# Optimization experiments

Hardware: AMD Instinct MI355X
Metric: run time of the kernel (lower is better)

## Reference

```python
import jax, jax.numpy as jnp
import numpy as np
from jax.scipy.linalg import expm

N = 2048

def setup_inputs() -> dict:
    key = jax.random.key(0)
    # Learnable parameter A, initialized as 0.01 * randn(n, n) per the module's __init__.
    A = 0.01 * jax.random.normal(key, (N, N), dtype=jnp.float32)
    return {"A": A}

def reference(A) -> jnp.ndarray:
    # S = A - A^T is skew-symmetric, so expm(S) lies in SO(n).
    S = A - A.T
    return expm(S)
```

## Files before the change

### kernel.cpp

```cpp
#include <hip/hip_runtime.h>
#include <stdint.h>

#define NM 2048

typedef _Float16 f16;
typedef __attribute__((ext_vector_type(8))) _Float16 half8;
typedef __attribute__((ext_vector_type(4))) float float4v;

__global__ void skew_f16_kernel(const float* __restrict__ A, f16* __restrict__ X) {
    __shared__ float t[32][33];
    const int bx = blockIdx.x * 32, by = blockIdx.y * 32;
    const int tx = threadIdx.x, ty = threadIdx.y;
    #pragma unroll
    for (int r = 0; r < 32; r += 8)
        t[ty + r][tx] = A[(size_t)(bx + ty + r) * NM + by + tx];
    __syncthreads();
    #pragma unroll
    for (int r = 0; r < 32; r += 8) {
        const int i = by + ty + r, j = bx + tx;
        X[(size_t)i * NM + j] = (f16)(A[(size_t)i * NM + j] - t[tx][ty + r]);
    }
}

template <int MODE>
__global__ __launch_bounds__(512, 4) void gemm_ps_kernel(
    const f16* __restrict__ Ap, const f16* __restrict__ BT,
    const f16* __restrict__ Xp, f16* __restrict__ X2p,
    f16* __restrict__ CTp, float* __restrict__ OUT) {
    constexpr int PLA = 128 * 64;
    constexpr int PLB = 64 * 64;
    constexpr int BUFH = PLA + PLB;
    constexpr int STAGEB = 2 * BUFH * 2;
    constexpr int MERGEB = 4 * 2176 * 4;
    constexpr int SMB = STAGEB > MERGEB ? STAGEB : MERGEB;
    __shared__ __align__(16) char smem_raw[SMB];

    const int tid = threadIdx.x;
    const int wave = tid >> 6, lane = tid & 63;
    const int grp = wave >> 2, w4 = wave & 3;
    const int wr = w4 >> 1, wc = w4 & 1;
    const int l15 = lane & 15, qq = lane >> 4;

    const int bid = blockIdx.x;
    const int xcd = bid & 7, li = bid >> 3;
    const int by = (xcd >> 2) * 8 + (li >> 3);
    const int bx = (xcd & 3) * 8 + (li & 7);
    const int rowBase = by * 128, colBase = bx * 64;

    const f16* gsrc[3];
    int ldsoff[3];
    #pragma unroll
    for (int u = 0; u < 3; ++u) {
        const int c = (u < 2) ? (u * 512 + tid) : tid;
        const int m = c >> 3, sp = c & 7;
        const int sl = sp ^ (m & 7);
        if (u < 2) {
            ldsoff[u] = c * 8;
            gsrc[u] = Ap + (size_t)(rowBase + m) * NM + sl * 8;
        } else {
            ldsoff[u] = PLA + c * 8;
            gsrc[u] = BT + (size_t)(colBase + m) * NM + sl * 8;
        }
    }

    int offA[4], offB[2];
    #pragma unroll
    for (int r = 0; r < 4; ++r) {
        const int m = wr * 64 + r * 16 + l15;
        offA[r] = (m * 8 + ((grp * 4 + qq) ^ (m & 7))) * 8;
    }
    #pragma unroll
    for (int c = 0; c < 2; ++c) {
        const int n = wc * 32 + c * 16 + l15;
        offB[c] = PLA + (n * 8 + ((grp * 4 + qq) ^ (n & 7))) * 8;
    }

    float4v acc[4][2];
    #pragma unroll
    for (int r = 0; r < 4; ++r)
        #pragma unroll
        for (int c = 0; c < 2; ++c)
            acc[r][c] = (float4v){0.f, 0.f, 0.f, 0.f};

    auto stage = [&](int buf) {
        f16* base = (f16*)smem_raw + buf * BUFH;
        #pragma unroll
        for (int u = 0; u < 3; ++u) {
            __builtin_amdgcn_global_load_lds(
                (const __attribute__((address_space(1))) void*)gsrc[u],
                (__attribute__((address_space(3))) void*)(uintptr_t)(base + ldsoff[u]),
                16, 0, 0);
            gsrc[u] += 64;
        }
    };

    stage(0);
    for (int k = 0; k < 32; ++k) {
        __syncthreads();
        if (k < 31) stage((k + 1) & 1);
        const f16* base = (const f16*)smem_raw + (k & 1) * BUFH;
        half8 ah[4], bh[2];
        #pragma unroll
        for (int r = 0; r < 4; ++r) ah[r] = *(const half8*)&base[offA[r]];
        #pragma unroll
        for (int c = 0; c < 2; ++c) bh[c] = *(const half8*)&base[offB[c]];
        #pragma unroll
        for (int r = 0; r < 4; ++r)
            #pragma unroll
            for (int c = 0; c < 2; ++c)
                acc[r][c] = __builtin_amdgcn_mfma_f32_16x16x32_f16(ah[r], bh[c], acc[r][c], 0, 0, 0);
    }

    __syncthreads();
    float* mbuf = (float*)smem_raw;
    if (wave >= 4) {
        float* base = mbuf + (size_t)w4 * 2176;
        #pragma unroll
        for (int r = 0; r < 4; ++r)
            #pragma unroll
            for (int c = 0; c < 2; ++c) {
                const int off = (c * 16 + l15) * 68 + r * 16 + qq * 4;
                *(float4v*)&base[off] = acc[r][c];
            }
    }
    __syncthreads();
    if (wave < 4) {
        const float* base = mbuf + (size_t)w4 * 2176;
        #pragma unroll
        for (int r = 0; r < 4; ++r)
            #pragma unroll
            for (int c = 0; c < 2; ++c) {
                const int off = (c * 16 + l15) * 68 + r * 16 + qq * 4;
                acc[r][c] += *(const float4v*)&base[off];
            }
        #pragma unroll
        for (int r = 0; r < 4; ++r)
            #pragma unroll
            for (int c = 0; c < 2; ++c)
                #pragma unroll
                for (int g = 0; g < 4; ++g) {
                    const int row = rowBase + wr * 64 + r * 16 + qq * 4 + g;
                    const int col = colBase + wc * 32 + c * 16 + l15;
                    const size_t off = (size_t)row * NM + col;
                    float v = acc[r][c][g];
                    if (MODE == 0) {
                        v = -v;
                        const float x = (float)Xp[off];
                        X2p[off] = (f16)v;
                        CTp[off] = (f16)(v * (256.0f / 24.0f) - x * (256.0f / 6.0f));
                    } else {
                        const float x = (float)Xp[off];
                        const float x2 = (float)X2p[off];
                        float o = x + 0.5f * x2 + v * (1.0f / 256.0f);
                        if (row == col) o += 1.0f;
                        OUT[off] = o;
                    }
                }
    }
}

extern "C" void kernel_launch(void* const* d_in, const int* in_sizes, int n_in,
                              void* d_out, int out_size, void* d_ws, size_t ws_size,
                              hipStream_t stream) {
    const float* A = (const float*)d_in[0];
    float* out = (float*)d_out;
    const size_t NN = (size_t)NM * NM;

    f16* X  = (f16*)d_ws;
    f16* X2 = X + NN;
    f16* CT = X2 + NN;

    dim3 tb(32, 8);
    dim3 tg(NM / 32, NM / 32);

    skew_f16_kernel<<<tg, tb, 0, stream>>>(A, X);
    gemm_ps_kernel<0><<<512, 512, 0, stream>>>(X, X, X, X2, CT, nullptr);
    gemm_ps_kernel<1><<<512, 512, 0, stream>>>(X2, CT, X, X2, nullptr, out);
}
```

Measured before the change: 124.0 us.

## Use 256x256 split-K GEMM tiles with partial sums and separate reduce kernels

New measurement: 136.2 us. +9.8%, slower.

```diff
diff --git a/kernel.cpp b/kernel.cpp
--- a/kernel.cpp
+++ b/kernel.cpp
@@ -22,141 +22,220 @@
     }
 }
 
-template <int MODE>
-__global__ __launch_bounds__(512, 4) void gemm_ps_kernel(
-    const f16* __restrict__ Ap, const f16* __restrict__ BT,
-    const f16* __restrict__ Xp, f16* __restrict__ X2p,
-    f16* __restrict__ CTp, float* __restrict__ OUT) {
-    constexpr int PLA = 128 * 64;
-    constexpr int PLB = 64 * 64;
-    constexpr int BUFH = PLA + PLB;
-    constexpr int STAGEB = 2 * BUFH * 2;
-    constexpr int MERGEB = 4 * 2176 * 4;
-    constexpr int SMB = STAGEB > MERGEB ? STAGEB : MERGEB;
-    __shared__ __align__(16) char smem_raw[SMB];
-
-    const int tid = threadIdx.x;
+#define STAGE_UNIT(kt, u)                                                         \
+    {                                                                             \
+        f16* _b = lds + ((kt) & 1) * BUFH;                                        \
+        const f16* _g = gsrc[u] + (kt) * 64;                                      \
+        __builtin_amdgcn_global_load_lds(                                         \
+            (const __attribute__((address_space(1))) void*)_g,                    \
+            (__attribute__((address_space(3))) void*)(uintptr_t)(_b + loff[u]),   \
+            16, 0, 0);                                                            \
+        __builtin_amdgcn_global_load_lds(                                         \
+            (const __attribute__((address_space(1))) void*)(_g + (size_t)128 * NM), \
+            (__attribute__((address_space(3))) void*)(uintptr_t)(_b + loff[u] + 8192), \
+            16, 0, 0);                                                            \
+    }
+
+#define MFMA_QUAD(MH, NH)                                                         \
+    __builtin_amdgcn_s_setprio(1);                                                \
+    _Pragma("unroll")                                                             \
+    for (int r = 0; r < 4; ++r)                                                   \
+        _Pragma("unroll")                                                         \
+        for (int c = 0; c < 2; ++c)                                               \
+            _Pragma("unroll")                                                     \
+            for (int kk = 0; kk < 2; ++kk)                                        \
+                acc[MH][NH][r][c] = __builtin_amdgcn_mfma_f32_16x16x32_f16(       \
+                    ah[r][kk], bh[c][kk], acc[MH][NH][r][c], 0, 0, 0);            \
+    __builtin_amdgcn_s_setprio(0);                                                \
+    asm volatile("s_waitcnt lgkmcnt(0)" ::: "memory");                            \
+    asm volatile("s_barrier" ::: "memory");
+
+__global__ __launch_bounds__(512, 2) void gemm8_kernel(
+    const f16* __restrict__ Ap, const f16* __restrict__ BTp, f16* __restrict__ Pp)
+{
+    extern __shared__ __align__(16) f16 lds[];
+    constexpr int PLB  = 16384;
+    constexpr int BUFH = 32768;
+    constexpr int NT   = 8;
+
+    const int tid  = threadIdx.x;
     const int wave = tid >> 6, lane = tid & 63;
-    const int grp = wave >> 2, w4 = wave & 3;
-    const int wr = w4 >> 1, wc = w4 & 1;
+    const int wr = wave >> 2, wc = wave & 3;
     const int l15 = lane & 15, qq = lane >> 4;
 
     const int bid = blockIdx.x;
     const int xcd = bid & 7, li = bid >> 3;
-    const int by = (xcd >> 2) * 8 + (li >> 3);
-    const int bx = (xcd & 3) * 8 + (li & 7);
-    const int rowBase = by * 128, colBase = bx * 64;
-
-    const f16* gsrc[3];
-    int ldsoff[3];
-    #pragma unroll
-    for (int u = 0; u < 3; ++u) {
-        const int c = (u < 2) ? (u * 512 + tid) : tid;
-        const int m = c >> 3, sp = c & 7;
-        const int sl = sp ^ (m & 7);
-        if (u < 2) {
-            ldsoff[u] = c * 8;
-            gsrc[u] = Ap + (size_t)(rowBase + m) * NM + sl * 8;
-        } else {
-            ldsoff[u] = PLA + c * 8;
-            gsrc[u] = BT + (size_t)(colBase + m) * NM + sl * 8;
+    const int sk   = xcd >> 1;
+    const int trow = (xcd & 1) * 4 + (li >> 3);
+    const int tcol = li & 7;
+    const int rowBase = trow * 256, colBase = tcol * 256;
+    const int kBase = sk * 512;
+
+    const f16* gsrc[4];
+    int loff[4];
+    {
+        const int m = tid >> 3, sp = tid & 7;
+        const int rA0 = m;
+        const int rA1 = 64 + m;
+        const int rB0 = (m & 31) + ((m >> 5) << 6);
+        const int rB1 = 32 + rB0;
+        gsrc[0] = Ap  + (size_t)(rowBase + rA0) * NM + kBase + (sp ^ (rA0 & 7)) * 8;
+        gsrc[1] = Ap  + (size_t)(rowBase + rA1) * NM + kBase + (sp ^ (rA1 & 7)) * 8;
+        gsrc[2] = BTp + (size_t)(colBase + rB0) * NM + kBase + (sp ^ (rB0 & 7)) * 8;
+        gsrc[3] = BTp + (size_t)(colBase + rB1) * NM + kBase + (sp ^ (rB1 & 7)) * 8;
+        loff[0] = (rA0 * 8 + sp) * 8;
+        loff[1] = (rA1 * 8 + sp) * 8;
+        loff[2] = PLB + (rB0 * 8 + sp) * 8;
+        loff[3] = PLB + (rB1 * 8 + sp) * 8;
+    }
+
+    int offA[4][2], offB[2][2];
+    #pragma unroll
+    for (int r = 0; r < 4; ++r)
+        #pragma unroll
+        for (int kk = 0; kk < 2; ++kk) {
+            const int row = wr * 128 + r * 16 + l15;
+            offA[r][kk] = (row * 8 + ((kk * 4 + qq) ^ (row & 7))) * 8;
         }
-    }
-
-    int offA[4], offB[2];
-    #pragma unroll
-    for (int r = 0; r < 4; ++r) {
-        const int m = wr * 64 + r * 16 + l15;
-        offA[r] = (m * 8 + ((grp * 4 + qq) ^ (m & 7))) * 8;
-    }
-    #pragma unroll
-    for (int c = 0; c < 2; ++c) {
-        const int n = wc * 32 + c * 16 + l15;
-        offB[c] = PLA + (n * 8 + ((grp * 4 + qq) ^ (n & 7))) * 8;
-    }
-
-    float4v acc[4][2];
-    #pragma unroll
-    for (int r = 0; r < 4; ++r)
+    #pragma unroll
+    for (int c = 0; c < 2; ++c)
+        #pragma unroll
+        for (int kk = 0; kk < 2; ++kk) {
+            const int row = wc * 64 + c * 16 + l15;
+            offB[c][kk] = PLB + (row * 8 + ((kk * 4 + qq) ^ (row & 7))) * 8;
+        }
+
+    float4v acc[2][2][4][2];
+    #pragma unroll
+    for (int mh = 0; mh < 2; ++mh)
+        #pragma unroll
+        for (int nh = 0; nh < 2; ++nh)
+            #pragma unroll
+            for (int r = 0; r < 4; ++r)
+                #pragma unroll
+                for (int c = 0; c < 2; ++c)
+                    acc[mh][nh][r][c] = (float4v){0.f, 0.f, 0.f, 0.f};
+
+    half8 ah[4][2], bh[2][2];
+
+    STAGE_UNIT(0, 0)
+    STAGE_UNIT(0, 3)
+    STAGE_UNIT(0, 1)
+    STAGE_UNIT(0, 2)
+    STAGE_UNIT(1, 0)
+    STAGE_UNIT(1, 3)
+
+    #pragma unroll
+    for (int t = 0; t < NT; ++t) {
+        const f16* base = lds + (t & 1) * BUFH;
+
+        if (t + 1 < NT) STAGE_UNIT(t + 1, 1)
+        if (t == NT - 1) { asm volatile("s_waitcnt vmcnt(0)" ::: "memory"); }
+        else             { asm volatile("s_waitcnt vmcnt(6)" ::: "memory"); }
+        asm volatile("s_barrier" ::: "memory");
+        #pragma unroll
+        for (int r = 0; r < 4; ++r)
+            #pragma unroll
+            for (int kk = 0; kk < 2; ++kk)
+                ah[r][kk] = *(const half8*)&base[offA[r][kk]];
         #pragma unroll
         for (int c = 0; c < 2; ++c)
-            acc[r][c] = (float4v){0.f, 0.f, 0.f, 0.f};
-
-    auto stage = [&](int buf) {
-        f16* base = (f16*)smem_raw + buf * BUFH;
-        #pragma unroll
-        for (int u = 0; u < 3; ++u) {
-            __builtin_amdgcn_global_load_lds(
-                (const __attribute__((address_space(1))) void*)gsrc[u],
-                (__attribute__((address_space(3))) void*)(uintptr_t)(base + ldsoff[u]),
-                16, 0, 0);
-            gsrc[u] += 64;
-        }
-    };
-
-    stage(0);
-    for (int k = 0; k < 32; ++k) {
-        __syncthreads();
-        if (k < 31) stage((k + 1) & 1);
-        const f16* base = (const f16*)smem_raw + (k & 1) * BUFH;
-        half8 ah[4], bh[2];
-        #pragma unroll
-        for (int r = 0; r < 4; ++r) ah[r] = *(const half8*)&base[offA[r]];
-        #pragma unroll
-        for (int c = 0; c < 2; ++c) bh[c] = *(const half8*)&base[offB[c]];
+            #pragma unroll
+            for (int kk = 0; kk < 2; ++kk)
+                bh[c][kk] = *(const half8*)&base[offB[c][kk]];
+        MFMA_QUAD(0, 0)
+
+        if (t + 1 < NT) STAGE_UNIT(t + 1, 2)
+        asm volatile("s_barrier" ::: "memory");
+        #pragma unroll
+        for (int c = 0; c < 2; ++c)
+            #pragma unroll
+            for (int kk = 0; kk < 2; ++kk)
+                bh[c][kk] = *(const half8*)&base[offB[c][kk] + 2048];
+        MFMA_QUAD(0, 1)
+
+        if (t + 2 < NT) STAGE_UNIT(t + 2, 0)
+        asm volatile("s_barrier" ::: "memory");
         #pragma unroll
         for (int r = 0; r < 4; ++r)
             #pragma unroll
-            for (int c = 0; c < 2; ++c)
-                acc[r][c] = __builtin_amdgcn_mfma_f32_16x16x32_f16(ah[r], bh[c], acc[r][c], 0, 0, 0);
-    }
-
-    __syncthreads();
-    float* mbuf = (float*)smem_raw;
-    if (wave >= 4) {
-        float* base = mbuf + (size_t)w4 * 2176;
-        #pragma unroll
-        for (int r = 0; r < 4; ++r)
-            #pragma unroll
-            for (int c = 0; c < 2; ++c) {
-                const int off = (c * 16 + l15) * 68 + r * 16 + qq * 4;
-                *(float4v*)&base[off] = acc[r][c];
-            }
-    }
-    __syncthreads();
-    if (wave < 4) {
-        const float* base = mbuf + (size_t)w4 * 2176;
-        #pragma unroll
-        for (int r = 0; r < 4; ++r)
-            #pragma unroll
-            for (int c = 0; c < 2; ++c) {
-                const int off = (c * 16 + l15) * 68 + r * 16 + qq * 4;
-                acc[r][c] += *(const float4v*)&base[off];
-            }
-        #pragma unroll
-        for (int r = 0; r < 4; ++r)
-            #pragma unroll
-            for (int c = 0; c < 2; ++c)
+            for (int kk = 0; kk < 2; ++kk)
+                ah[r][kk] = *(const half8*)&base[offA[r][kk] + 4096];
+        MFMA_QUAD(1, 1)
+
+        if (t + 2 < NT) STAGE_UNIT(t + 2, 3)
+        asm volatile("s_barrier" ::: "memory");
+        #pragma unroll
+        for (int c = 0; c < 2; ++c)
+            #pragma unroll
+            for (int kk = 0; kk < 2; ++kk)
+                bh[c][kk] = *(const half8*)&base[offB[c][kk]];
+        MFMA_QUAD(1, 0)
+    }
+
+    f16* dst = Pp + (size_t)sk * NM * NM;
+    #pragma unroll
+    for (int mh = 0; mh < 2; ++mh)
+        #pragma unroll
+        for (int nh = 0; nh < 2; ++nh)
+            #pragma unroll
+            for (int r = 0; r < 4; ++r)
                 #pragma unroll
-                for (int g = 0; g < 4; ++g) {
-                    const int row = rowBase + wr * 64 + r * 16 + qq * 4 + g;
-                    const int col = colBase + wc * 32 + c * 16 + l15;
-                    const size_t off = (size_t)row * NM + col;
-                    float v = acc[r][c][g];
-                    if (MODE == 0) {
-                        v = -v;
-                        const float x = (float)Xp[off];
-                        X2p[off] = (f16)v;
-                        CTp[off] = (f16)(v * (256.0f / 24.0f) - x * (256.0f / 6.0f));
-                    } else {
-                        const float x = (float)Xp[off];
-                        const float x2 = (float)X2p[off];
-                        float o = x + 0.5f * x2 + v * (1.0f / 256.0f);
-                        if (row == col) o += 1.0f;
-                        OUT[off] = o;
+                for (int c = 0; c < 2; ++c)
+                    #pragma unroll
+                    for (int g = 0; g < 4; ++g) {
+                        const int row = rowBase + wr * 128 + mh * 64 + r * 16 + qq * 4 + g;
+                        const int col = colBase + wc * 64 + nh * 32 + c * 16 + l15;
+                        dst[(size_t)row * NM + col] = (f16)acc[mh][nh][r][c][g];
                     }
-                }
-    }
+}
+
+__global__ __launch_bounds__(256) void reduce0_kernel(
+    const f16* __restrict__ P, const f16* __restrict__ X,
+    f16* __restrict__ X2, f16* __restrict__ CT)
+{
+    const size_t NN = (size_t)NM * NM;
+    const size_t i = ((size_t)blockIdx.x * 256 + threadIdx.x) * 8;
+    const half8 p0 = *(const half8*)(P + i);
+    const half8 p1 = *(const half8*)(P + NN + i);
+    const half8 p2 = *(const half8*)(P + 2 * NN + i);
+    const half8 p3 = *(const half8*)(P + 3 * NN + i);
+    const half8 xv = *(const half8*)(X + i);
+    half8 x2v, ctv;
+    #pragma unroll
+    for (int j = 0; j < 8; ++j) {
+        const float s  = (float)p0[j] + (float)p1[j] + (float)p2[j] + (float)p3[j];
+        const float x2 = -s;
+        const float x  = (float)xv[j];
+        x2v[j] = (f16)x2;
+        ctv[j] = (f16)(x2 * (256.0f / 24.0f) - x * (256.0f / 6.0f));
+    }
+    *(half8*)(X2 + i) = x2v;
+    *(half8*)(CT + i) = ctv;
+}
+
+__global__ __launch_bounds__(256) void reduce1_kernel(
+    const f16* __restrict__ P, const f16* __restrict__ X,
+    const f16* __restrict__ X2, float* __restrict__ OUT)
+{
+    const size_t NN = (size_t)NM * NM;
+    const size_t i = ((size_t)blockIdx.x * 256 + threadIdx.x) * 8;
+    const half8 p0  = *(const half8*)(P + i);
+    const half8 p1  = *(const half8*)(P + NN + i);
+    const half8 p2  = *(const half8*)(P + 2 * NN + i);
+    const half8 p3  = *(const half8*)(P + 3 * NN + i);
+    const half8 xv  = *(const half8*)(X + i);
+    const half8 x2v = *(const half8*)(X2 + i);
+    float o[8];
+    #pragma unroll
+    for (int j = 0; j < 8; ++j) {
+        const float q = (float)p0[j] + (float)p1[j] + (float)p2[j] + (float)p3[j];
+        o[j] = (float)xv[j] + 0.5f * (float)x2v[j] + q * (1.0f / 256.0f);
+    }
+    const int row = (int)(i >> 11), col0 = (int)(i & 2047);
+    if (row >= col0 && row < col0 + 8) o[row - col0] += 1.0f;
+    *(float4v*)(OUT + i)     = (float4v){o[0], o[1], o[2], o[3]};
+    *(float4v*)(OUT + i + 4) = (float4v){o[4], o[5], o[6], o[7]};
 }
 
 extern "C" void kernel_launch(void* const* d_in, const int* in_sizes, int n_in,
@@ -169,11 +248,19 @@
     f16* X  = (f16*)d_ws;
     f16* X2 = X + NN;
     f16* CT = X2 + NN;
-
-    dim3 tb(32, 8);
-    dim3 tg(NM / 32, NM / 32);
-
+    f16* P  = CT + NN;
+
+    static int attr_done = 0;
+    if (!attr_done) {
+        hipFuncSetAttribute((const void*)gemm8_kernel,
+                            hipFuncAttributeMaxDynamicSharedMemorySize, 131072);
+        attr_done = 1;
+    }
+
+    dim3 tb(32, 8), tg(NM / 32, NM / 32);
     skew_f16_kernel<<<tg, tb, 0, stream>>>(A, X);
-    gemm_ps_kernel<0><<<512, 512, 0, stream>>>(X, X, X, X2, CT, nullptr);
-    gemm_ps_kernel<1><<<512, 512, 0, stream>>>(X2, CT, X, X2, nullptr, out);
-}
+    gemm8_kernel<<<256, 512, 131072, stream>>>(X, X, P);
+    reduce0_kernel<<<2048, 256, 0, stream>>>(P, X, X2, CT);
+    gemm8_kernel<<<256, 512, 131072, stream>>>(X2, CT, P);
+    reduce1_kernel<<<2048, 256, 0, stream>>>(P, X, X2, out);
+}
```

## Restructure GEMM to 128x128 tiles with explicit half-tile LDS pipelining

Applied to the files above, without the earlier changes.

Measured after the change: 122.7 us. No clear change (-1.1%).

```diff
diff --git a/kernel.cpp b/kernel.cpp
--- a/kernel.cpp
+++ b/kernel.cpp
@@ -22,141 +22,172 @@
     }
 }
 
+#define BARRIER asm volatile("s_barrier" ::: "memory")
+#define LG0     asm volatile("s_waitcnt lgkmcnt(0)" ::: "memory")
+#define W3      asm volatile("s_waitcnt vmcnt(3)" ::: "memory")
+#define W0      asm volatile("s_waitcnt vmcnt(0)" ::: "memory")
+#define NOST    ((void)0)
+
+#define STAGE_1(u, dst)                                                       \
+    do {                                                                      \
+        __builtin_amdgcn_global_load_lds(                                     \
+            (const __attribute__((address_space(1))) void*)gsrc[u],           \
+            (__attribute__((address_space(3))) void*)(uintptr_t)((dst) + loff[u]), \
+            16, 0, 0);                                                        \
+        gsrc[u] += 64;                                                        \
+    } while (0)
+
+#define RD_A(BB, HOFF)                                                       \
+    { _Pragma("unroll")                                                      \
+      for (int r_ = 0; r_ < 2; ++r_)                                         \
+        _Pragma("unroll")                                                    \
+        for (int k_ = 0; k_ < 2; ++k_)                                       \
+            ah[r_][k_] = *(const half8*)&(BB)[offA[r_][k_] + (HOFF)]; }
+
+#define RD_B(BB)                                                             \
+    { _Pragma("unroll")                                                      \
+      for (int c_ = 0; c_ < 2; ++c_)                                         \
+        _Pragma("unroll")                                                    \
+        for (int k_ = 0; k_ < 2; ++k_)                                       \
+            bh[c_][k_] = *(const half8*)&(BB)[offB[c_][k_]]; }
+
+#define MPH(MH)                                                              \
+    __builtin_amdgcn_s_setprio(1);                                           \
+    _Pragma("unroll")                                                        \
+    for (int r_ = 0; r_ < 2; ++r_)                                           \
+        _Pragma("unroll")                                                    \
+        for (int c_ = 0; c_ < 2; ++c_)                                       \
+            _Pragma("unroll")                                                 \
+            for (int k_ = 0; k_ < 2; ++k_)                                   \
+                acc[MH][r_][c_] = __builtin_amdgcn_mfma_f32_16x16x32_f16(    \
+                    ah[r_][k_], bh[c_][k_], acc[MH][r_][c_], 0, 0, 0);       \
+    __builtin_amdgcn_s_setprio(0);
+
+#define TILE2(CUR, S1, S2, WEND)                                             \
+    {                                                                        \
+        const f16* Bb = (CUR);                                               \
+                                                  \
+        RD_A(Bb, 0); RD_B(Bb);                                               \
+        S1;                                                                  \
+        BARRIER; LG0;                                                        \
+        MPH(0);                                                              \
+        BARRIER;                                                             \
+                                  \
+        RD_A(Bb, 2048);                                                      \
+        S2;                                                                  \
+        BARRIER; LG0;                                                        \
+        MPH(1);                                                              \
+        WEND; BARRIER;                                                       \
+    }
+
 template <int MODE>
-__global__ __launch_bounds__(512, 4) void gemm_ps_kernel(
-    const f16* __restrict__ Ap, const f16* __restrict__ BT,
+__global__ __launch_bounds__(512, 1) void gemm_fused_kernel(
+    const f16* __restrict__ Ap, const f16* __restrict__ BTp,
     const f16* __restrict__ Xp, f16* __restrict__ X2p,
-    f16* __restrict__ CTp, float* __restrict__ OUT) {
-    constexpr int PLA = 128 * 64;
-    constexpr int PLB = 64 * 64;
-    constexpr int BUFH = PLA + PLB;
-    constexpr int STAGEB = 2 * BUFH * 2;
-    constexpr int MERGEB = 4 * 2176 * 4;
-    constexpr int SMB = STAGEB > MERGEB ? STAGEB : MERGEB;
-    __shared__ __align__(16) char smem_raw[SMB];
-
-    const int tid = threadIdx.x;
+    f16* __restrict__ CTp, float* __restrict__ OUT)
+{
+    extern __shared__ __align__(16) f16 lds[];
+    constexpr int PLB  = 8192;
+    constexpr int BUFH = 16384;
+
+    const int tid  = threadIdx.x;
     const int wave = tid >> 6, lane = tid & 63;
-    const int grp = wave >> 2, w4 = wave & 3;
-    const int wr = w4 >> 1, wc = w4 & 1;
+    const int wr = wave >> 2, wc = wave & 3;
     const int l15 = lane & 15, qq = lane >> 4;
 
     const int bid = blockIdx.x;
     const int xcd = bid & 7, li = bid >> 3;
-    const int by = (xcd >> 2) * 8 + (li >> 3);
-    const int bx = (xcd & 3) * 8 + (li & 7);
-    const int rowBase = by * 128, colBase = bx * 64;
-
-    const f16* gsrc[3];
-    int ldsoff[3];
-    #pragma unroll
-    for (int u = 0; u < 3; ++u) {
-        const int c = (u < 2) ? (u * 512 + tid) : tid;
-        const int m = c >> 3, sp = c & 7;
-        const int sl = sp ^ (m & 7);
-        if (u < 2) {
-            ldsoff[u] = c * 8;
-            gsrc[u] = Ap + (size_t)(rowBase + m) * NM + sl * 8;
-        } else {
-            ldsoff[u] = PLA + c * 8;
-            gsrc[u] = BT + (size_t)(colBase + m) * NM + sl * 8;
+    const int trow = (xcd & 3) * 4 + (li >> 3);
+    const int tcol = (xcd >> 2) * 8 + (li & 7);
+    const int rowBase = trow * 128, colBase = tcol * 128;
+
+    const f16* gsrc[4];
+    int loff[4];
+    {
+        const int m = tid >> 3, sp = tid & 7;
+        const int rA0 = (m & 31) + ((m >> 5) << 6);
+        const int rA1 = 32 + rA0;
+        const int rB0 = m;
+        const int rB1 = 64 + m;
+        gsrc[0] = Ap  + (size_t)(rowBase + rA0) * NM + (sp ^ (rA0 & 7)) * 8;
+        gsrc[1] = Ap  + (size_t)(rowBase + rA1) * NM + (sp ^ (rA1 & 7)) * 8;
+        gsrc[2] = BTp + (size_t)(colBase + rB0) * NM + (sp ^ (rB0 & 7)) * 8;
+        gsrc[3] = BTp + (size_t)(colBase + rB1) * NM + (sp ^ (rB1 & 7)) * 8;
+        loff[0] = (rA0 * 8 + sp) * 8;
+        loff[1] = (rA1 * 8 + sp) * 8;
+        loff[2] = PLB + (rB0 * 8 + sp) * 8;
+        loff[3] = PLB + (rB1 * 8 + sp) * 8;
+    }
+
+    int offA[2][2], offB[2][2];
+    #pragma unroll
+    for (int r = 0; r < 2; ++r)
+        #pragma unroll
+        for (int kk = 0; kk < 2; ++kk) {
+            const int row = wr * 64 + r * 16 + l15;
+            offA[r][kk] = (row * 8 + ((kk * 4 + qq) ^ (row & 7))) * 8;
         }
-    }
-
-    int offA[4], offB[2];
-    #pragma unroll
-    for (int r = 0; r < 4; ++r) {
-        const int m = wr * 64 + r * 16 + l15;
-        offA[r] = (m * 8 + ((grp * 4 + qq) ^ (m & 7))) * 8;
-    }
-    #pragma unroll
-    for (int c = 0; c < 2; ++c) {
-        const int n = wc * 32 + c * 16 + l15;
-        offB[c] = PLA + (n * 8 + ((grp * 4 + qq) ^ (n & 7))) * 8;
-    }
-
-    float4v acc[4][2];
-    #pragma unroll
-    for (int r = 0; r < 4; ++r)
-        #pragma unroll
-        for (int c = 0; c < 2; ++c)
-            acc[r][c] = (float4v){0.f, 0.f, 0.f, 0.f};
-
-    auto stage = [&](int buf) {
-        f16* base = (f16*)smem_raw + buf * BUFH;
-        #pragma unroll
-        for (int u = 0; u < 3; ++u) {
-            __builtin_amdgcn_global_load_lds(
-                (const __attribute__((address_space(1))) void*)gsrc[u],
-                (__attribute__((address_space(3))) void*)(uintptr_t)(base + ldsoff[u]),
-                16, 0, 0);
-            gsrc[u] += 64;
+    #pragma unroll
+    for (int c = 0; c < 2; ++c)
+        #pragma unroll
+        for (int kk = 0; kk < 2; ++kk) {
+            const int row = wc * 32 + c * 16 + l15;
+            offB[c][kk] = PLB + (row * 8 + ((kk * 4 + qq) ^ (row & 7))) * 8;
         }
-    };
-
-    stage(0);
-    for (int k = 0; k < 32; ++k) {
-        __syncthreads();
-        if (k < 31) stage((k + 1) & 1);
-        const f16* base = (const f16*)smem_raw + (k & 1) * BUFH;
-        half8 ah[4], bh[2];
-        #pragma unroll
-        for (int r = 0; r < 4; ++r) ah[r] = *(const half8*)&base[offA[r]];
-        #pragma unroll
-        for (int c = 0; c < 2; ++c) bh[c] = *(const half8*)&base[offB[c]];
-        #pragma unroll
-        for (int r = 0; r < 4; ++r)
+
+    float4v acc[2][2][2];
+    #pragma unroll
+    for (int mh = 0; mh < 2; ++mh)
+        #pragma unroll
+        for (int r = 0; r < 2; ++r)
             #pragma unroll
             for (int c = 0; c < 2; ++c)
-                acc[r][c] = __builtin_amdgcn_mfma_f32_16x16x32_f16(ah[r], bh[c], acc[r][c], 0, 0, 0);
-    }
-
-    __syncthreads();
-    float* mbuf = (float*)smem_raw;
-    if (wave >= 4) {
-        float* base = mbuf + (size_t)w4 * 2176;
-        #pragma unroll
-        for (int r = 0; r < 4; ++r)
-            #pragma unroll
-            for (int c = 0; c < 2; ++c) {
-                const int off = (c * 16 + l15) * 68 + r * 16 + qq * 4;
-                *(float4v*)&base[off] = acc[r][c];
-            }
-    }
-    __syncthreads();
-    if (wave < 4) {
-        const float* base = mbuf + (size_t)w4 * 2176;
-        #pragma unroll
-        for (int r = 0; r < 4; ++r)
-            #pragma unroll
-            for (int c = 0; c < 2; ++c) {
-                const int off = (c * 16 + l15) * 68 + r * 16 + qq * 4;
-                acc[r][c] += *(const float4v*)&base[off];
-            }
-        #pragma unroll
-        for (int r = 0; r < 4; ++r)
+                acc[mh][r][c] = (float4v){0.f, 0.f, 0.f, 0.f};
+
+    half8 ah[2][2], bh[2][2];
+
+    f16* B0 = lds;
+    f16* B1 = lds + BUFH;
+
+    STAGE_1(0, B0); STAGE_1(1, B0); STAGE_1(2, B0); STAGE_1(3, B0);
+    STAGE_1(0, B1); STAGE_1(2, B1); STAGE_1(3, B1);
+    W3; BARRIER;
+
+    #pragma unroll 1
+    for (int i = 0; i < 15; ++i) {
+        TILE2(B0, STAGE_1(1, B1),
+              { STAGE_1(0, B0); STAGE_1(2, B0); STAGE_1(3, B0); }, W3)
+        TILE2(B1, STAGE_1(1, B0),
+              { STAGE_1(0, B1); STAGE_1(2, B1); STAGE_1(3, B1); }, W3)
+    }
+    TILE2(B0, STAGE_1(1, B1), NOST, W0)
+    TILE2(B1, NOST, NOST, NOST)
+
+    #pragma unroll
+    for (int mh = 0; mh < 2; ++mh)
+        #pragma unroll
+        for (int r = 0; r < 2; ++r)
             #pragma unroll
             for (int c = 0; c < 2; ++c)
                 #pragma unroll
                 for (int g = 0; g < 4; ++g) {
-                    const int row = rowBase + wr * 64 + r * 16 + qq * 4 + g;
+                    const int row = rowBase + wr * 64 + mh * 32 + r * 16 + qq * 4 + g;
                     const int col = colBase + wc * 32 + c * 16 + l15;
                     const size_t off = (size_t)row * NM + col;
-                    float v = acc[r][c][g];
+                    const float p = acc[mh][r][c][g];
                     if (MODE == 0) {
-                        v = -v;
+                        const float v = -p;
                         const float x = (float)Xp[off];
                         X2p[off] = (f16)v;
                         CTp[off] = (f16)(v * (256.0f / 24.0f) - x * (256.0f / 6.0f));
                     } else {
-                        const float x = (float)Xp[off];
+                        const float x  = (float)Xp[off];
                         const float x2 = (float)X2p[off];
-                        float o = x + 0.5f * x2 + v * (1.0f / 256.0f);
+                        float o = x + 0.5f * x2 + p * (1.0f / 256.0f);
                         if (row == col) o += 1.0f;
                         OUT[off] = o;
                     }
                 }
-    }
 }
 
 extern "C" void kernel_launch(void* const* d_in, const int* in_sizes, int n_in,
@@ -170,10 +201,17 @@
     f16* X2 = X + NN;
     f16* CT = X2 + NN;
 
-    dim3 tb(32, 8);
-    dim3 tg(NM / 32, NM / 32);
-
+    static int attr_done = 0;
+    if (!attr_done) {
+        hipFuncSetAttribute((const void*)gemm_fused_kernel<0>,
+                            hipFuncAttributeMaxDynamicSharedMemorySize, 65536);
+        hipFuncSetAttribute((const void*)gemm_fused_kernel<1>,
+                            hipFuncAttributeMaxDynamicSharedMemorySize, 65536);
+        attr_done = 1;
+    }
+
+    dim3 tb(32, 8), tg(NM / 32, NM / 32);
     skew_f16_kernel<<<tg, tb, 0, stream>>>(A, X);
-    gemm_ps_kernel<0><<<512, 512, 0, stream>>>(X, X, X, X2, CT, nullptr);
-    gemm_ps_kernel<1><<<512, 512, 0, stream>>>(X2, CT, X, X2, nullptr, out);
+    gemm_fused_kernel<0><<<256, 512, 65536, stream>>>(X, X, X, X2, CT, nullptr);
+    gemm_fused_kernel<1><<<256, 512, 65536, stream>>>(X2, CT, X, X2, nullptr, out);
 }
```
